# Kernel tuning notes

Measured on AMD Instinct MI355X. Metric: run time of the kernel, lower is better.

Reference implementation:

```python
import jax, jax.numpy as jnp
import numpy as np

TOP_K = 2


def setup_inputs() -> dict:
    key = jax.random.key(0)
    kx, kw = jax.random.split(key)
    B, S, D, E = 4, 4096, 4096, 16
    x = jax.random.normal(kx, (B, S, D), dtype=jnp.float32)
    W = jax.random.normal(kw, (E, D), dtype=jnp.float32) * (1.0 / np.sqrt(D))
    b = jnp.zeros((E,), dtype=jnp.float32)
    return {"x": x, "W": W, "b": b}


def reference(x, W, b):
    B, S, D = x.shape
    E = W.shape[0]
    T = B * S  # total tokens
    x_flat = x.reshape(T, D)

    # router linear: (T, D) @ (D, E) + b
    router_logits = jnp.einsum("td,ed->te", x_flat, W) + b
    router_probs = jax.nn.softmax(router_logits, axis=-1)

    # top-k selection and renormalization
    top_k_probs, top_k_indices = jax.lax.top_k(router_probs, TOP_K)
    top_k_probs = top_k_probs / jnp.sum(top_k_probs, axis=-1, keepdims=True)

    # one-hot dispatch tensor via scatter (indices within a row are unique)
    token_ids = jnp.arange(T)[:, None]  # (T, 1) broadcast against (T, k)
    dispatch_tensor = jnp.zeros_like(router_probs).at[token_ids, top_k_indices].set(top_k_probs)

    # per-expert token index lists (jit-compatible padded form).
    # Row e holds the sorted token indices routed to expert e, padded with -1.
    mask = dispatch_tensor > 0  # (T, E)
    counts = jnp.sum(mask, axis=0)  # (E,)
    # stable argsort of ~mask puts assigned-token indices first, in order
    order = jnp.argsort(~mask.T, axis=1)  # (E, T), stable by default
    expert_indices = jnp.where(jnp.arange(T)[None, :] < counts[:, None], order, -1)

    return router_logits, dispatch_tensor, expert_indices
```

## Files before the change

kernel.cpp:

```cpp
#include <hip/hip_runtime.h>
#include <cstdint>
#include <cstddef>

#define DDIM 4096
#define D4   1024
#define NE   16
#define KC4  128
#define NCHUNK 8
#define SCHUNK 256

__device__ __forceinline__ void load_lds16(const void* g, void* l) {
    __builtin_amdgcn_global_load_lds(
        (const __attribute__((address_space(1))) unsigned int*)g,
        (__attribute__((address_space(3))) unsigned int*)l, 16, 0, 0);
}

__device__ __forceinline__ float dot4(float4 a, float4 w) {
    return a.x * w.x + a.y * w.y + a.z * w.z + a.w * w.w;
}

__global__ __launch_bounds__(256, 2) void router_pass_a(
    const float* __restrict__ x, const float* __restrict__ W,
    const float* __restrict__ b, float* __restrict__ out,
    unsigned char* __restrict__ packed, int* __restrict__ gcounts, int T)
{
    __shared__ float4 shW4[2 * NE * KC4];

    const int tid  = (int)threadIdx.x;
    const int lane = tid & 63;
    const int wid  = tid >> 6;
    const int tg   = lane >> 4;
    const int kl   = lane & 15;
    const int tok0 = ((int)blockIdx.x * 4 + wid) * 8 + tg * 2;

    const float4* __restrict__ x4 = (const float4*)x;
    const float4* __restrict__ W4 = (const float4*)W;
    const float4* xr0 = x4 + (size_t)tok0 * D4;
    const float4* xr1 = xr0 + D4;

    float acc0[NE], acc1[NE];
#pragma unroll
    for (int e = 0; e < NE; ++e) { acc0[e] = 0.f; acc1[e] = 0.f; }

#pragma unroll
    for (int j = 0; j < 8; ++j) {
        const int slot = wid * 8 + j;
        const int e = slot >> 1, half = slot & 1;
        load_lds16((const void*)(W4 + (size_t)e * D4 + half * 64 + lane),
                   (void*)(shW4 + slot * 64));
    }

    for (int kc = 0; kc < NCHUNK; ++kc) {
        __syncthreads();

        if (kc < NCHUNK - 1) {
            const int nb = ((kc + 1) & 1) * (NE * KC4);
#pragma unroll
            for (int j = 0; j < 8; ++j) {
                const int slot = wid * 8 + j;
                const int e = slot >> 1, half = slot & 1;
                load_lds16((const void*)(W4 + (size_t)e * D4 + (kc + 1) * KC4 +
                                         half * 64 + lane),
                           (void*)(shW4 + nb + slot * 64));
            }
        }

        const float4* bufp = shW4 + (kc & 1) * (NE * KC4);
        const int base = kc * KC4;
#pragma unroll 2
        for (int i = 0; i < 8; ++i) {
            const int f = base + kl + (i << 4);
            float4 a0 = xr0[f];
            float4 a1 = xr1[f];
            const float4* wrow = bufp + kl + (i << 4);
#pragma unroll
            for (int e = 0; e < NE; ++e) {
                float4 w = wrow[e * KC4];
                acc0[e] += dot4(a0, w);
                acc1[e] += dot4(a1, w);
            }
        }
    }

#pragma unroll
    for (int m = 8; m >= 1; m >>= 1) {
        const bool hi = (kl & m) != 0;
#pragma unroll
        for (int j = 0; j < m; ++j) {
            float s0 = hi ? acc0[j] : acc0[j + m];
            float k0 = hi ? acc0[j + m] : acc0[j];
            acc0[j] = k0 + __shfl_xor(s0, m, 64);
            float s1 = hi ? acc1[j] : acc1[j + m];
            float k1 = hi ? acc1[j + m] : acc1[j];
            acc1[j] = k1 + __shfl_xor(s1, m, 64);
        }
    }

    const float logit0 = acc0[0] + b[kl];
    const float logit1 = acc1[0] + b[kl];
    out[(size_t)tok0 * NE + kl]       = logit0;
    out[(size_t)(tok0 + 1) * NE + kl] = logit1;

    float m1a = logit0; int i1a = kl; float m2a = -__builtin_inff(); int i2a = NE;
    float m1b = logit1; int i1b = kl; float m2b = -__builtin_inff(); int i2b = NE;
#pragma unroll
    for (int m = 1; m <= 8; m <<= 1) {
        {
            float om1 = __shfl_xor(m1a, m, 64); int oi1 = __shfl_xor(i1a, m, 64);
            float om2 = __shfl_xor(m2a, m, 64); int oi2 = __shfl_xor(i2a, m, 64);
            bool aF = (m1a > om1) || (m1a == om1 && i1a < oi1);
            float n1v = aF ? m1a : om1; int n1i = aF ? i1a : oi1;
            float l1v = aF ? om1 : m1a; int l1i = aF ? oi1 : i1a;
            float c2v = aF ? m2a : om2; int c2i = aF ? i2a : oi2;
            bool s = (l1v > c2v) || (l1v == c2v && l1i < c2i);
            m1a = n1v; i1a = n1i; m2a = s ? l1v : c2v; i2a = s ? l1i : c2i;
        }
        {
            float om1 = __shfl_xor(m1b, m, 64); int oi1 = __shfl_xor(i1b, m, 64);
            float om2 = __shfl_xor(m2b, m, 64); int oi2 = __shfl_xor(i2b, m, 64);
            bool aF = (m1b > om1) || (m1b == om1 && i1b < oi1);
            float n1v = aF ? m1b : om1; int n1i = aF ? i1b : oi1;
            float l1v = aF ? om1 : m1b; int l1i = aF ? oi1 : i1b;
            float c2v = aF ? m2b : om2; int c2i = aF ? i2b : oi2;
            bool s = (l1v > c2v) || (l1v == c2v && l1i < c2i);
            m1b = n1v; i1b = n1i; m2b = s ? l1v : c2v; i2b = s ? l1i : c2i;
        }
    }

    float* __restrict__ disp = out + (size_t)T * NE;
    {
        const float q = expf(m2a - m1a);
        const float r1 = 1.f / (1.f + q), r2 = q / (1.f + q);
        disp[(size_t)tok0 * NE + kl] = (kl == i1a) ? r1 : ((kl == i2a) ? r2 : 0.f);
    }
    {
        const float q = expf(m2b - m1b);
        const float r1 = 1.f / (1.f + q), r2 = q / (1.f + q);
        disp[(size_t)(tok0 + 1) * NE + kl] = (kl == i1b) ? r1 : ((kl == i2b) ? r2 : 0.f);
    }

    if (kl == 0) {
        packed[tok0]     = (unsigned char)(i1a | (i2a << 4));
        packed[tok0 + 1] = (unsigned char)(i1b | (i2b << 4));
        int* gc = gcounts + (size_t)(tok0 >> 8) * NE;
        atomicAdd(&gc[i1a], 1);
        atomicAdd(&gc[i2a], 1);
        atomicAdd(&gc[i1b], 1);
        atomicAdd(&gc[i2b], 1);
    }
}

__global__ __launch_bounds__(256) void router_fill(
    float* __restrict__ idxout, int* __restrict__ gcounts)
{
    const int t = (int)(blockIdx.x * 256 + threadIdx.x);
    float4* o4 = (float4*)idxout;
    o4[t] = make_float4(-1.f, -1.f, -1.f, -1.f);
    if (t < (16384 / SCHUNK) * NE) gcounts[t] = 0;
}

__global__ __launch_bounds__(SCHUNK) void router_scatter(
    const unsigned char* __restrict__ packed, const int* __restrict__ gcounts,
    float* __restrict__ idxout, int T)
{
    const int c    = (int)blockIdx.x;
    const int tid  = (int)threadIdx.x;
    const int lane = tid & 63;
    const int wid  = tid >> 6;
    __shared__ int offs[NE];
    __shared__ int wtot[SCHUNK / 64][NE];

    if (tid < NE) offs[tid] = 0;
    __syncthreads();
    {
        const int e = tid & 15, j = tid >> 4;
        int s = 0;
        for (int cc = j; cc < c; cc += 16) s += gcounts[cc * NE + e];
        if (s) atomicAdd(&offs[e], s);
    }

    const int t = c * SCHUNK + tid;
    const unsigned p = packed[t];
    const int e1 = (int)(p & 15);
    const int e2 = (int)(p >> 4);

    unsigned long long bal[NE];
#pragma unroll
    for (int ee = 0; ee < NE; ++ee)
        bal[ee] = __ballot((e1 == ee) || (e2 == ee));

    if (lane < NE) wtot[wid][lane] = __popcll(bal[lane]);
    __syncthreads();

    const unsigned long long lt = (1ull << lane) - 1ull;
    int r1 = __popcll(bal[e1] & lt);
    int r2 = __popcll(bal[e2] & lt);
    for (int w = 0; w < wid; ++w) { r1 += wtot[w][e1]; r2 += wtot[w][e2]; }

    idxout[(size_t)e1 * T + offs[e1] + r1] = (float)t;
    idxout[(size_t)e2 * T + offs[e2] + r2] = (float)t;
}

extern "C" void kernel_launch(void* const* d_in, const int* in_sizes, int n_in,
                              void* d_out, int out_size, void* d_ws, size_t ws_size,
                              hipStream_t stream)
{
    const float* x = (const float*)d_in[0];
    const float* W = (const float*)d_in[1];
    const float* b = (const float*)d_in[2];
    float* out = (float*)d_out;

    const int T = in_sizes[0] / DDIM;

    unsigned char* packed = (unsigned char*)d_ws;
    int* gcounts = (int*)((char*)d_ws + (((size_t)T + 255) & ~(size_t)255));

    float* idxout = out + (size_t)2 * T * NE;

    router_fill<<<(NE * T / 4) / 256, 256, 0, stream>>>(idxout, gcounts);

    router_pass_a<<<T / 32, 256, 0, stream>>>(x, W, b, out, packed, gcounts, T);

    router_scatter<<<T / SCHUNK, SCHUNK, 0, stream>>>(packed, gcounts, idxout, T);
}
```

Measured before the change: 372.3 us.

## Software-pipeline x loads in router GEMV and fold -1 fill into main kernel

```diff
diff --git a/kernel.cpp b/kernel.cpp
--- a/kernel.cpp
+++ b/kernel.cpp
@@ -22,7 +22,8 @@
 __global__ __launch_bounds__(256, 2) void router_pass_a(
     const float* __restrict__ x, const float* __restrict__ W,
     const float* __restrict__ b, float* __restrict__ out,
-    unsigned char* __restrict__ packed, int* __restrict__ gcounts, int T)
+    unsigned char* __restrict__ packed, int* __restrict__ gcounts,
+    float* __restrict__ idxout, int T)
 {
     __shared__ float4 shW4[2 * NE * KC4];
 
@@ -35,8 +36,8 @@
 
     const float4* __restrict__ x4 = (const float4*)x;
     const float4* __restrict__ W4 = (const float4*)W;
-    const float4* xr0 = x4 + (size_t)tok0 * D4;
-    const float4* xr1 = xr0 + D4;
+    const float4* xp0 = x4 + (size_t)tok0 * D4 + kl;
+    const float4* xp1 = xp0 + D4;
 
     float acc0[NE], acc1[NE];
 #pragma unroll
@@ -49,6 +50,14 @@
         load_lds16((const void*)(W4 + (size_t)e * D4 + half * 64 + lane),
                    (void*)(shW4 + slot * 64));
     }
+
+    if (tid < 128)
+        ((float4*)idxout)[(size_t)blockIdx.x * 128 + tid] =
+            make_float4(-1.f, -1.f, -1.f, -1.f);
+
+    float4 A0[4], A1[4], B0[4], B1[4];
+#pragma unroll
+    for (int i = 0; i < 4; ++i) { A0[i] = xp0[i << 4]; A1[i] = xp1[i << 4]; }
 
     for (int kc = 0; kc < NCHUNK; ++kc) {
         __syncthreads();
@@ -65,19 +74,38 @@
             }
         }
 
-        const float4* bufp = shW4 + (kc & 1) * (NE * KC4);
-        const int base = kc * KC4;
-#pragma unroll 2
-        for (int i = 0; i < 8; ++i) {
-            const int f = base + kl + (i << 4);
-            float4 a0 = xr0[f];
-            float4 a1 = xr1[f];
-            const float4* wrow = bufp + kl + (i << 4);
-#pragma unroll
-            for (int e = 0; e < NE; ++e) {
-                float4 w = wrow[e * KC4];
-                acc0[e] += dot4(a0, w);
-                acc1[e] += dot4(a1, w);
+        const float4* bufp = shW4 + (kc & 1) * (NE * KC4) + kl;
+        const float4* xb0 = xp0 + kc * KC4;
+        const float4* xb1 = xp1 + kc * KC4;
+
+#pragma unroll
+        for (int i = 0; i < 4; ++i) {
+            B0[i] = xb0[64 + (i << 4)];
+            B1[i] = xb1[64 + (i << 4)];
+        }
+#pragma unroll
+        for (int e = 0; e < NE; ++e) {
+#pragma unroll
+            for (int i = 0; i < 4; ++i) {
+                float4 w = bufp[e * KC4 + (i << 4)];
+                acc0[e] += dot4(A0[i], w);
+                acc1[e] += dot4(A1[i], w);
+            }
+        }
+        if (kc < NCHUNK - 1) {
+#pragma unroll
+            for (int i = 0; i < 4; ++i) {
+                A0[i] = xb0[KC4 + (i << 4)];
+                A1[i] = xb1[KC4 + (i << 4)];
+            }
+        }
+#pragma unroll
+        for (int e = 0; e < NE; ++e) {
+#pragma unroll
+            for (int i = 0; i < 4; ++i) {
+                float4 w = bufp[e * KC4 + 64 + (i << 4)];
+                acc0[e] += dot4(B0[i], w);
+                acc1[e] += dot4(B1[i], w);
             }
         }
     }
@@ -150,13 +178,12 @@
     }
 }
 
-__global__ __launch_bounds__(256) void router_fill(
-    float* __restrict__ idxout, int* __restrict__ gcounts)
-{
-    const int t = (int)(blockIdx.x * 256 + threadIdx.x);
-    float4* o4 = (float4*)idxout;
-    o4[t] = make_float4(-1.f, -1.f, -1.f, -1.f);
-    if (t < (16384 / SCHUNK) * NE) gcounts[t] = 0;
+__global__ __launch_bounds__(256) void router_zero(
+    int* __restrict__ gcounts, int n4)
+{
+    int4* g4 = (int4*)gcounts;
+    for (int i = (int)threadIdx.x; i < n4; i += 256)
+        g4[i] = make_int4(0, 0, 0, 0);
 }
 
 __global__ __launch_bounds__(SCHUNK) void router_scatter(
@@ -217,9 +244,10 @@
 
     float* idxout = out + (size_t)2 * T * NE;
 
-    router_fill<<<(NE * T / 4) / 256, 256, 0, stream>>>(idxout, gcounts);
-
-    router_pass_a<<<T / 32, 256, 0, stream>>>(x, W, b, out, packed, gcounts, T);
+    router_zero<<<1, 256, 0, stream>>>(gcounts, (T / SCHUNK) * NE / 4);
+
+    router_pass_a<<<T / 32, 256, 0, stream>>>(x, W, b, out, packed, gcounts,
+                                              idxout, T);
 
     router_scatter<<<T / SCHUNK, SCHUNK, 0, stream>>>(packed, gcounts, idxout, T);
 }
```

After: 590.7 us. 1.59x slower.
